# Kernel tuning notes

Measured on AMD Instinct MI355X. Metric: run time of the kernel, lower is better.

## Reference

```python
import jax, jax.numpy as jnp
import numpy as np

B, C, N, K, G = 4, 128, 4096, 9, 4


def setup_inputs() -> dict:
    key = jax.random.key(0)
    ks = jax.random.split(key, 4)
    s = 0.05
    return {
        "features": jax.random.normal(ks[0], (B, C, N, 1), jnp.float32),
        # Attn.linear: Conv2d(2C -> C, 1x1)
        "w_lin": jax.random.normal(ks[1], (C, 2 * C), jnp.float32) * s,
        "b_lin": jnp.zeros((C,), jnp.float32),
        # atten_weight_conv: Linear(C -> K*G)
        "w_aw": jax.random.normal(ks[2], (K * G, C), jnp.float32) * s,
        "b_aw": jnp.zeros((K * G,), jnp.float32),
        # GroupNorm(4, C)
        "gn_g": jnp.ones((C,), jnp.float32),
        "gn_b": jnp.zeros((C,), jnp.float32),
        # conv: Conv2d(C -> C, 1x1) + BatchNorm2d(C)
        "conv_w": jax.random.normal(ks[3], (C, C), jnp.float32) * s,
        "conv_b": jnp.zeros((C,), jnp.float32),
        "bn_g": jnp.ones((C,), jnp.float32),
        "bn_b": jnp.zeros((C,), jnp.float32),
    }


def reference(features, w_lin, b_lin, w_aw, b_aw, gn_g, gn_b, conv_w, conv_b, bn_g, bn_b):
    B, C, N, _ = features.shape
    K, G = 9, 4
    Cg = C // G  # 32 channels per group
    EPS = 1e-5

    x = features[..., 0]                       # [B,C,N]
    # ---- KNN graph (negative squared distance, top-k) ----
    xx = jnp.sum(x * x, axis=1)                # [B,N]
    inner = jnp.einsum('bcn,bcm->bnm', x, x)   # [B,N,N]
    pd = 2.0 * inner - xx[:, :, None] - xx[:, None, :]
    idx = jax.lax.top_k(pd, K)[1]              # [B,N,K]

    # ---- edge feature gather: cat(x, x - x_neighbor) ----
    xt = x.transpose(0, 2, 1)                  # [B,N,C]
    b_ix = jnp.arange(B)[:, None, None]
    nbr = xt[b_ix, idx]                        # [B,N,K,C]
    ctr = jnp.broadcast_to(xt[:, :, None, :], (B, N, K, C))
    edge = jnp.concatenate([ctr, ctr - nbr], axis=-1)   # [B,N,K,2C]

    # ---- Attn.linear (1x1 conv == per-position linear) ----
    feat = jnp.einsum('bnke,ce->bnkc', edge, w_lin) + b_lin  # [B,N,K,C]

    # ---- grouped channel attention (4 groups of 32) ----
    fg = feat.reshape(B, N, K, G, Cg)
    scores = jnp.einsum('bnkgc,bnjgc->bngkj', fg, fg) / np.sqrt(32.0)
    s = jax.nn.softmax(scores, axis=-1)        # [B,N,G,K,K]
    attn = jnp.einsum('bngkj,bnjgc->bngkc', s, jax.nn.elu(fg))  # [B,N,G,K,Cg]

    # ---- attention weights over neighbors ----
    aw = jnp.einsum('bnc,dc->bnd', xt, w_aw) + b_aw          # [B,N,K*G]
    aw = jax.nn.softmax(aw.reshape(B, N, G, K), axis=-1)     # [B,N,G,K]

    # ---- weighted neighbor combine ----
    lf = jnp.einsum('bngk,bngkc->bngc', aw, attn)            # [B,N,G,Cg]
    lf = lf.transpose(0, 2, 3, 1).reshape(B, C, N, 1)        # [B,C,N,1]

    # ---- GroupNorm(4, C) over residual ----
    y = lf + features
    yg = y.reshape(B, G, Cg * N)
    mu = yg.mean(-1, keepdims=True)
    var = yg.var(-1, keepdims=True)
    yn = ((yg - mu) / jnp.sqrt(var + EPS)).reshape(B, C, N, 1)
    yn = yn * gn_g[None, :, None, None] + gn_b[None, :, None, None]

    # ---- 1x1 conv + BatchNorm (training-mode batch stats) + ReLU ----
    z = jnp.einsum('oc,bcnk->bonk', conv_w, yn) + conv_b[None, :, None, None]
    m = z.mean(axis=(0, 2, 3), keepdims=True)
    v = z.var(axis=(0, 2, 3), keepdims=True)
    z = (z - m) / jnp.sqrt(v + EPS) * bn_g[None, :, None, None] + bn_b[None, :, None, None]
    return jax.nn.relu(z)
```

## Files before the change

kernel.cpp:

```cpp
#include <hip/hip_runtime.h>
#include <hip/hip_bf16.h>
#include <cstddef>

#define NPTS 4096
#define CCH  128
#define KNN  9
#define GRP  4
#define BB   4
#define OFF_XT    0u
#define OFF_XX    2097152u
#define OFF_XHI   2113536u
#define OFF_IDX   3162112u
#define OFF_O     3309568u
#define OFF_Y     8159232u
#define OFF_GNP   10256384u
#define OFF_GNA   10387456u
#define OFF_GND   10387968u
#define OFF_WP    10388480u
#define OFF_BIASP 10454016u
#define OFF_BNSUM 10454528u
#define OFF_BNSQ  10454656u
#define OFF_BNSC  10454784u
#define OFF_BNSH  10454912u

using bf16x8 = __attribute__((ext_vector_type(8))) short;
using f32x4  = __attribute__((ext_vector_type(4))) float;

#define CE(a, b) { float _h = fmaxf(a, b); b = fminf(a, b); a = _h; }

#define BMERGE16(s) \
  CE(s[0],s[8])  CE(s[1],s[9])  CE(s[2],s[10]) CE(s[3],s[11]) \
  CE(s[4],s[12]) CE(s[5],s[13]) CE(s[6],s[14]) CE(s[7],s[15]) \
  CE(s[0],s[4])  CE(s[1],s[5])  CE(s[2],s[6])  CE(s[3],s[7])  \
  CE(s[8],s[12]) CE(s[9],s[13]) CE(s[10],s[14]) CE(s[11],s[15]) \
  CE(s[0],s[2])  CE(s[1],s[3])  CE(s[4],s[6])  CE(s[5],s[7])  \
  CE(s[8],s[10]) CE(s[9],s[11]) CE(s[12],s[14]) CE(s[13],s[15]) \
  CE(s[0],s[1])  CE(s[2],s[3])  CE(s[4],s[5])  CE(s[6],s[7])  \
  CE(s[8],s[9])  CE(s[10],s[11]) CE(s[12],s[13]) CE(s[14],s[15])

#define SENT_BITS 0xFF7FF000u

__global__ void k_transpose(const float* __restrict__ x, float* __restrict__ xt,
                            __hip_bfloat16* __restrict__ xhi, float* __restrict__ xx) {
  __shared__ float t[32][33];
  int tx = threadIdx.x, ty = threadIdx.y;
  int n0 = blockIdx.x * 32, c0 = blockIdx.y * 32, b = blockIdx.z;
  float v = x[((size_t)b * CCH + c0 + ty) * NPTS + n0 + tx];
  t[ty][tx] = v;
  __syncthreads();
  float tv = t[tx][ty];
  size_t R = (size_t)b * NPTS + n0 + ty;
  int c = c0 + tx;
  xt[R * CCH + c] = tv;
  int g = c >> 3, w = c & 7;
  int sc = (((g ^ ((n0 + ty) & 15)) << 3) | w);
  xhi[R * CCH + sc] = __float2bfloat16(tv);
  if (ty == 0) {
    float s = 0.f;
    #pragma unroll
    for (int k = 0; k < 32; k++) { float u = t[k][tx]; s += u * u; }
    atomicAdd(&xx[b * NPTS + n0 + tx], s);
  }
}

__device__ __forceinline__ void select_chunk(int c, int wave, int quad,
                                             const f32x4 (&acc)[2][2],
                                             float (&top8)[2][8]) {
  const unsigned cbase = (unsigned)(c * 128 + wave * 32 + quad * 4);
  #pragma unroll
  for (int qt = 0; qt < 2; qt++) {
    float k[8];
    #pragma unroll
    for (int ct = 0; ct < 2; ct++)
      #pragma unroll
      for (int r = 0; r < 4; r++) {
        unsigned u = __float_as_uint(acc[ct][qt][r]);
        k[ct * 4 + r] = __uint_as_float((u & 0xFFFFF000u) |
                                        (cbase + (unsigned)(ct * 16 + r)));
      }
    CE(k[0],k[1]) CE(k[2],k[3]) CE(k[4],k[5]) CE(k[6],k[7])
    CE(k[0],k[2]) CE(k[1],k[3]) CE(k[4],k[6]) CE(k[5],k[7])
    CE(k[1],k[2]) CE(k[5],k[6])
    CE(k[0],k[4]) CE(k[1],k[5]) CE(k[2],k[6]) CE(k[3],k[7])
    CE(k[2],k[4]) CE(k[3],k[5])
    CE(k[1],k[2]) CE(k[3],k[4]) CE(k[5],k[6])
    float t[8];
    #pragma unroll
    for (int i = 0; i < 8; i++) t[i] = fmaxf(top8[qt][i], k[7 - i]);
    CE(t[0],t[4]) CE(t[1],t[5]) CE(t[2],t[6]) CE(t[3],t[7])
    CE(t[0],t[2]) CE(t[1],t[3]) CE(t[4],t[6]) CE(t[5],t[7])
    CE(t[0],t[1]) CE(t[2],t[3]) CE(t[4],t[5]) CE(t[6],t[7])
    #pragma unroll
    for (int i = 0; i < 8; i++) top8[qt][i] = t[i];
  }
}

__device__ __forceinline__ void load_chunk(const short* __restrict__ xb,
                                           const int (&aoff)[4], int c,
                                           bf16x8 (&af)[2][4]) {
  const short* cb = xb + c * (128 * CCH);
  #pragma unroll
  for (int ks = 0; ks < 4; ks++) {
    af[0][ks] = *(const bf16x8*)(cb + aoff[ks]);
    af[1][ks] = *(const bf16x8*)(cb + 2048 + aoff[ks]);
  }
}

__launch_bounds__(256, 4)
__global__ void k_knn(const short* __restrict__ xhi, const float* __restrict__ xx,
                      float* __restrict__ cand) {
  __shared__ short Qs[32 * 136];
  __shared__ float XXs[2048];
  const int tid = threadIdx.x;
  const int wave = tid >> 6, lane = tid & 63;
  const int quad = lane >> 4, m = lane & 15;
  const int b = blockIdx.y;
  const int q0 = blockIdx.x * 32;
  const int z = blockIdx.z;
  const int ch0 = z * 16;
  const short* xb = xhi + (size_t)b * NPTS * CCH;
  const float* xxb = xx + (b << 12);

  {
    int f = tid;
    #pragma unroll
    for (int it = 0; it < 2; it++, f += 256) {
      int row = f >> 4, s = f & 15;
      bf16x8 v = *(const bf16x8*)(xb + (size_t)(q0 + row) * CCH + s * 8);
      int g = s ^ (row & 15);
      *(bf16x8*)&Qs[row * 136 + g * 8] = v;
    }
    const float4* src4 = (const float4*)(xxb + ch0 * 128);
    float4* dst4 = (float4*)XXs;
    #pragma unroll
    for (int j = 0; j < 2; j++) {
      float4 v = src4[tid * 2 + j];
      dst4[tid * 2 + j] = make_float4(-0.5f * v.x, -0.5f * v.y, -0.5f * v.z, -0.5f * v.w);
    }
  }

  int aoff[4];
  #pragma unroll
  for (int ks = 0; ks < 4; ks++)
    aoff[ks] = (wave * 32 + m) * CCH + (((ks * 4 + quad) ^ m) * 8);

  float top8[2][8];
  #pragma unroll
  for (int qt = 0; qt < 2; qt++)
    #pragma unroll
    for (int p = 0; p < 8; p++) top8[qt][p] = __uint_as_float(SENT_BITS);

  f32x4 acc[2][2];
  bf16x8 bufA[2][4], bufB[2][4];

  unsigned qoff = (unsigned)(m * 272 + quad * 16);
  const unsigned xbase = (unsigned)(wave * 128 + quad * 16);

  load_chunk(xb, aoff, ch0, bufA);
  __syncthreads();

  auto mfma_lds = [&](const bf16x8 (&af)[2][4], int crel) {
    unsigned xo = xbase + (unsigned)crel * 512u;
    f32x4 ci0 = *(const f32x4*)((const char*)XXs + xo);
    f32x4 ci1 = *(const f32x4*)((const char*)XXs + xo + 64);
    acc[0][0] = ci0; acc[0][1] = ci0; acc[1][0] = ci1; acc[1][1] = ci1;
    #pragma unroll
    for (int ks = 0; ks < 4; ks++) {
      bf16x8 qv0 = *(const bf16x8*)((const char*)Qs + qoff + ks * 64);
      bf16x8 qv1 = *(const bf16x8*)((const char*)Qs + qoff + 4352 + ks * 64);
      acc[0][0] = __builtin_amdgcn_mfma_f32_16x16x32_bf16(af[0][ks], qv0, acc[0][0], 0, 0, 0);
      acc[0][1] = __builtin_amdgcn_mfma_f32_16x16x32_bf16(af[0][ks], qv1, acc[0][1], 0, 0, 0);
      acc[1][0] = __builtin_amdgcn_mfma_f32_16x16x32_bf16(af[1][ks], qv0, acc[1][0], 0, 0, 0);
      acc[1][1] = __builtin_amdgcn_mfma_f32_16x16x32_bf16(af[1][ks], qv1, acc[1][1], 0, 0, 0);
    }
  };

  for (int c = ch0; c < ch0 + 16; c += 2) {
    load_chunk(xb, aoff, c + 1, bufB);
    if (c > ch0) select_chunk(c - 1, wave, quad, acc, top8);
    asm volatile("" : "+v"(qoff));
    mfma_lds(bufA, c - ch0);
    if (c + 2 < ch0 + 16) load_chunk(xb, aoff, c + 2, bufA);
    select_chunk(c, wave, quad, acc, top8);
    asm volatile("" : "+v"(qoff));
    mfma_lds(bufB, c + 1 - ch0);
  }
  select_chunk(ch0 + 15, wave, quad, acc, top8);

  #pragma unroll
  for (int qt = 0; qt < 2; qt++) {
    float s[16];
    #pragma unroll
    for (int i = 0; i < 8; i++) {
      s[i] = top8[qt][i];
      s[15 - i] = __shfl_xor(top8[qt][i], 16);
    }
    BMERGE16(s)
    float t[16];
    #pragma unroll
    for (int i = 0; i < 16; i++) t[i] = fmaxf(s[i], __shfl_xor(s[15 - i], 32));
    BMERGE16(t)
    if (quad == 0) {
      int q = q0 + qt * 16 + m;
      float* dst = cand + ((size_t)((b << 12) + q) * 128 + (size_t)(z * 4 + wave) * 16);
      *(float4*)&dst[0]  = make_float4(t[0],  t[1],  t[2],  t[3]);
      *(float4*)&dst[4]  = make_float4(t[4],  t[5],  t[6],  t[7]);
      *(float4*)&dst[8]  = make_float4(t[8],  t[9],  t[10], t[11]);
      *(float4*)&dst[12] = make_float4(t[12], t[13], t[14], t[15]);
    }
  }
}

__launch_bounds__(256)
__global__ void k_rerank(const float* __restrict__ cand, const float* __restrict__ xt,
                         const float* __restrict__ xx, int* __restrict__ idxOut) {
  __shared__ __align__(16) float runS[4][128];
  __shared__ int selS[4][16];
  __shared__ float keyS[4][16];
  int tid = threadIdx.x, wave = tid >> 6, lane = tid & 63;
  int qg = blockIdx.x * 4 + wave;
  int b = qg >> 12;
  const float* src = cand + (size_t)qg * 128;
  if (lane < 32) *(float4*)&runS[wave][lane * 4] = *(const float4*)&src[lane * 4];
  __syncthreads();
  if (lane < 16) {
    float t = runS[wave][lane];
    #pragma unroll
    for (int r = 1; r < 8; r++) {
      t = fmaxf(t, runS[wave][r * 16 + (15 - lane)]);
      #pragma unroll
      for (int d = 8; d >= 1; d >>= 1) {
        float o = __shfl_xor(t, d);
        t = (lane & d) ? fminf(t, o) : fmaxf(t, o);
      }
    }
    selS[wave][lane] = (int)(__float_as_uint(t) & 0xFFFu);
  }
  __syncthreads();
  int cnum = lane >> 2, part = lane & 3;
  int cidx = selS[wave][cnum];
  const float* rq = xt + (size_t)qg * CCH;
  const float* rc = xt + ((size_t)(b << 12) + cidx) * CCH;
  float dot = 0.f;
  #pragma unroll
  for (int j = 0; j < 8; j++) {
    float4 a4 = *(const float4*)&rq[part * 32 + j * 4];
    float4 c4 = *(const float4*)&rc[part * 32 + j * 4];
    dot += a4.x * c4.x + a4.y * c4.y + a4.z * c4.z + a4.w * c4.w;
  }
  dot += __shfl_xor(dot, 1);
  dot += __shfl_xor(dot, 2);
  if (part == 0)
    keyS[wave][cnum] = fmaf(2.f, dot, -xx[(b << 12) + cidx]);
  __syncthreads();
  if (lane < 16) {
    float k = keyS[wave][lane]; int i = selS[wave][lane];
    int r = 0;
    #pragma unroll
    for (int f = 0; f < 16; f++) {
      float fk = keyS[wave][f]; int fi = selS[wave][f];
      r += (fk > k) || (fk == k && fi < i);
    }
    if (r < 9) idxOut[(size_t)qg * 9 + r] = i;
  }
}

__launch_bounds__(256)
__global__ void k_linear(const float* __restrict__ xt, const float* __restrict__ w_lin,
                         const float* __restrict__ b_lin, const float* __restrict__ w_aw,
                         const float* __restrict__ b_aw, float* __restrict__ O) {
  __shared__ __align__(16) float Xs[64 * 132];
  __shared__ __align__(16) float Ws[64 * 132];
  int tid = threadIdx.x;
  int tx = tid & 15, ty = tid >> 4;
  int p0 = blockIdx.x * 64, o0 = blockIdx.y * 64;
  #pragma unroll
  for (int i = 0; i < 8; i++) {
    int flat = tid + i * 256; int r = flat >> 5, c4 = flat & 31;
    *(float4*)&Xs[r * 132 + c4 * 4] = *(const float4*)&xt[(size_t)(p0 + r) * CCH + c4 * 4];
  }
  #pragma unroll
  for (int i = 0; i < 8; i++) {
    int flat = tid + i * 256; int r = flat >> 5, c4 = flat & 31;
    int o = o0 + r; float4 v;
    if (o < 128) {
      float4 a = *(const float4*)&w_lin[(size_t)o * 256 + c4 * 4];
      float4 c = *(const float4*)&w_lin[(size_t)o * 256 + 128 + c4 * 4];
      v = make_float4(a.x + c.x, a.y + c.y, a.z + c.z, a.w + c.w);
    } else if (o < 256) {
      v = *(const float4*)&w_lin[(size_t)(o - 128) * 256 + 128 + c4 * 4];
    } else if (o < 292) {
      v = *(const float4*)&w_aw[(size_t)(o - 256) * 128 + c4 * 4];
    } else v = make_float4(0.f, 0.f, 0.f, 0.f);
    *(float4*)&Ws[r * 132 + c4 * 4] = v;
  }
  __syncthreads();
  float acc[4][4] = {};
  #pragma unroll 2
  for (int kq = 0; kq < 32; kq++) {
    float4 xa[4], wb[4];
    #pragma unroll
    for (int i = 0; i < 4; i++) xa[i] = *(const float4*)&Xs[(ty * 4 + i) * 132 + kq * 4];
    #pragma unroll
    for (int j = 0; j < 4; j++) wb[j] = *(const float4*)&Ws[(tx + 16 * j) * 132 + kq * 4];
    #pragma unroll
    for (int i = 0; i < 4; i++)
      #pragma unroll
      for (int j = 0; j < 4; j++)
        acc[i][j] += xa[i].x * wb[j].x + xa[i].y * wb[j].y + xa[i].z * wb[j].z + xa[i].w * wb[j].w;
  }
  #pragma unroll
  for (int j = 0; j < 4; j++) {
    int o = o0 + tx + 16 * j;
    if (o < 292) {
      float bias = (o < 128) ? b_lin[o] : ((o < 256) ? 0.f : b_aw[o - 256]);
      #pragma unroll
      for (int i = 0; i < 4; i++)
        O[(size_t)(p0 + ty * 4 + i) * 296 + o] = acc[i][j] + bias;
    }
  }
}

__launch_bounds__(256)
__global__ void k_attn(const float* __restrict__ O, const int* __restrict__ idxArr,
                       const float* __restrict__ xt, float* __restrict__ Y,
                       float* __restrict__ gnPart) {
  __shared__ __align__(16) float fF[4][1188];
  __shared__ __align__(16) float scS[4][432];
  __shared__ float awS[4][48];
  __shared__ float w9S[4][48];
  __shared__ int tI[45], tJ[45];
  int tid = threadIdx.x;
  int wave = tid >> 6, l = tid & 63;
  int pos = blockIdx.x * 4 + wave;
  int b = pos >> 12;
  if (tid == 0) {
    int p = 0;
    for (int i = 0; i < 9; i++) for (int j = i; j < 9; j++) { tI[p] = i; tJ[p] = j; p++; }
  }
  int nbr[9];
  const float* Op = O + (size_t)pos * 296;
  #pragma unroll
  for (int k = 0; k < 9; k++) nbr[k] = idxArr[(size_t)pos * 9 + k];
  float2 u = *(const float2*)(Op + 2 * l);
  float* fFw = fF[wave];
  #pragma unroll
  for (int k = 0; k < 9; k++) {
    const float* vp = O + (size_t)((b << 12) + nbr[k]) * 296 + 128;
    float2 vv = *(const float2*)(vp + 2 * l);
    *(float2*)&fFw[k * 132 + 2 * l] = make_float2(u.x - vv.x, u.y - vv.y);
  }
  __syncthreads();
  #pragma unroll
  for (int r = 0; r < 3; r++) {
    int p = r * 64 + l;
    if (p < 180) {
      int g = p / 45, q = p - g * 45;
      int i = tI[q], j = tJ[q];
      const float* fi = fFw + i * 132 + g * 32;
      const float* fj = fFw + j * 132 + g * 32;
      float s = 0.f;
      #pragma unroll
      for (int t8 = 0; t8 < 8; t8++) {
        float4 a4 = *(const float4*)(fi + 4 * t8);
        float4 b4 = *(const float4*)(fj + 4 * t8);
        s += a4.x * b4.x + a4.y * b4.y + a4.z * b4.z + a4.w * b4.w;
      }
      s *= 0.17677669529663687f;
      scS[wave][(g * 9 + i) * 12 + j] = s;
      scS[wave][(g * 9 + j) * 12 + i] = s;
    }
  }
  __syncthreads();
  if (l < 36) {
    int g = l / 9, i = l - g * 9;
    float* rp = &scS[wave][(g * 9 + i) * 12];
    float mx = rp[0];
    #pragma unroll
    for (int j = 1; j < 9; j++) mx = fmaxf(mx, rp[j]);
    float e[9]; float sm = 0.f;
    #pragma unroll
    for (int j = 0; j < 9; j++) { e[j] = __expf(rp[j] - mx); sm += e[j]; }
    float inv = 1.f / sm;
    #pragma unroll
    for (int j = 0; j < 9; j++) rp[j] = e[j] * inv;
  } else if (l < 40) {
    int g = l - 36;
    float a[9]; float mx = -3.4e38f;
    #pragma unroll
    for (int k = 0; k < 9; k++) { a[k] = Op[256 + g * 9 + k]; mx = fmaxf(mx, a[k]); }
    float sm = 0.f;
    #pragma unroll
    for (int k = 0; k < 9; k++) { a[k] = __expf(a[k] - mx); sm += a[k]; }
    float inv = 1.f / sm;
    #pragma unroll
    for (int k = 0; k < 9; k++) awS[wave][g * 12 + k] = a[k] * inv;
  }
  __syncthreads();
  if (l < 36) {
    int g = l / 9, j = l - g * 9;
    float s = 0.f;
    #pragma unroll
    for (int i = 0; i < 9; i++) s += awS[wave][g * 12 + i] * scS[wave][(g * 9 + i) * 12 + j];
    w9S[wave][g * 12 + j] = s;
  }
  __syncthreads();
  int g = l >> 4;
  float w9r[9];
  #pragma unroll
  for (int j = 0; j < 9; j++) w9r[j] = w9S[wave][g * 12 + j];
  int c0 = 2 * l;
  float lf0 = 0.f, lf1 = 0.f;
  #pragma unroll
  for (int j = 0; j < 9; j++) {
    float2 f2 = *(const float2*)&fFw[j * 132 + c0];
    float e0 = f2.x > 0.f ? f2.x : __expf(f2.x) - 1.f;
    float e1 = f2.y > 0.f ? f2.y : __expf(f2.y) - 1.f;
    lf0 += w9r[j] * e0;
    lf1 += w9r[j] * e1;
  }
  float2 xv = *(const float2*)(xt + (size_t)pos * CCH + c0);
  float y0 = lf0 + xv.x, y1 = lf1 + xv.y;
  *(float2*)(Y + (size_t)pos * CCH + c0) = make_float2(y0, y1);
  float s1 = y0 + y1, s2 = y0 * y0 + y1 * y1;
  #pragma unroll
  for (int mm = 1; mm <= 8; mm <<= 1) { s1 += __shfl_xor(s1, mm); s2 += __shfl_xor(s2, mm); }
  if ((l & 15) == 0) {
    gnPart[(size_t)pos * 8 + g * 2]     = s1;
    gnPart[(size_t)pos * 8 + g * 2 + 1] = s2;
  }
}

__global__ void k_gnstats(const float* __restrict__ gnPart,
                          const float* __restrict__ gn_g, const float* __restrict__ gn_b,
                          float* __restrict__ gnA, float* __restrict__ gnD) {
  int bg = blockIdx.x; int b = bg >> 2, g = bg & 3;
  int tid = threadIdx.x;
  float s1 = 0.f, s2 = 0.f;
  for (int r = tid; r < NPTS; r += 256) {
    const float* p = gnPart + (size_t)(b * NPTS + r) * 8 + g * 2;
    s1 += p[0]; s2 += p[1];
  }
  __shared__ float r1[256], r2[256];
  r1[tid] = s1; r2[tid] = s2;
  __syncthreads();
  for (int off = 128; off > 0; off >>= 1) {
    if (tid < off) { r1[tid] += r1[tid + off]; r2[tid] += r2[tid + off]; }
    __syncthreads();
  }
  __shared__ float muS, rsS;
  if (tid == 0) {
    float mu = r1[0] * (1.f / 131072.f);
    float var = r2[0] * (1.f / 131072.f) - mu * mu;
    muS = mu; rsS = 1.f / sqrtf(var + 1e-5f);
  }
  __syncthreads();
  if (tid < 32) {
    int c = g * 32 + tid;
    float a = rsS * gn_g[c];
    gnA[b * 128 + c] = a;
    gnD[b * 128 + c] = gn_b[c] - muS * a;
  }
}

__global__ void k_fold(const float* __restrict__ conv_w, const float* __restrict__ conv_b,
                       const float* __restrict__ gnA, const float* __restrict__ gnD,
                       float* __restrict__ Wp, float* __restrict__ biasp) {
  int b = blockIdx.x; int tid = threadIdx.x;
  __shared__ float dS[128], aS[128];
  if (tid < 128) { dS[tid] = gnD[b * 128 + tid]; aS[tid] = gnA[b * 128 + tid]; }
  __syncthreads();
  for (int f = tid; f < 16384; f += 256)
    Wp[(size_t)b * 16384 + f] = conv_w[f] * aS[f & 127];
  if (tid < 128) {
    float s = conv_b[tid];
    for (int c = 0; c < 128; c++) s += conv_w[tid * 128 + c] * dS[c];
    biasp[b * 128 + tid] = s;
  }
}

__launch_bounds__(256)
__global__ void k_conv(const float* __restrict__ Y, const float* __restrict__ Wp,
                       const float* __restrict__ biasp, float* __restrict__ zpre,
                       float* __restrict__ bnSum, float* __restrict__ bnSq) {
  __shared__ __align__(16) float Ys[64 * 132];
  __shared__ __align__(16) float Ws[64 * 132];
  int tid = threadIdx.x;
  int tx = tid & 15, ty = tid >> 4;
  int n0 = blockIdx.x * 64, o0 = blockIdx.y * 64, b = blockIdx.z;
  #pragma unroll
  for (int i = 0; i < 8; i++) {
    int flat = tid + i * 256; int r = flat >> 5, c4 = flat & 31;
    *(float4*)&Ys[r * 132 + c4 * 4] = *(const float4*)&Y[(size_t)((b << 12) + n0 + r) * CCH + c4 * 4];
    *(float4*)&Ws[r * 132 + c4 * 4] = *(const float4*)&Wp[(size_t)b * 16384 + (size_t)(o0 + r) * 128 + c4 * 4];
  }
  __syncthreads();
  float acc[4][4] = {};
  #pragma unroll 2
  for (int kq = 0; kq < 32; kq++) {
    float4 wa[4], yb[4];
    #pragma unroll
    for (int i = 0; i < 4; i++) wa[i] = *(const float4*)&Ws[(ty * 4 + i) * 132 + kq * 4];
    #pragma unroll
    for (int j = 0; j < 4; j++) yb[j] = *(const float4*)&Ys[(tx + 16 * j) * 132 + kq * 4];
    #pragma unroll
    for (int i = 0; i < 4; i++)
      #pragma unroll
      for (int j = 0; j < 4; j++)
        acc[i][j] += wa[i].x * yb[j].x + wa[i].y * yb[j].y + wa[i].z * yb[j].z + wa[i].w * yb[j].w;
  }
  #pragma unroll
  for (int i = 0; i < 4; i++) {
    int o = o0 + ty * 4 + i;
    float bias = biasp[b * 128 + o];
    float p1 = 0.f, p2 = 0.f;
    #pragma unroll
    for (int j = 0; j < 4; j++) {
      float z = acc[i][j] + bias;
      zpre[(((size_t)((b << 7) + o)) << 12) + n0 + tx + 16 * j] = z;
      p1 += z; p2 += z * z;
    }
    #pragma unroll
    for (int mm = 1; mm <= 8; mm <<= 1) { p1 += __shfl_xor(p1, mm); p2 += __shfl_xor(p2, mm); }
    if (tx == 0) { atomicAdd(&bnSum[o], p1); atomicAdd(&bnSq[o], p2); }
  }
}

__global__ void k_bnfin(const float* __restrict__ bnSum, const float* __restrict__ bnSq,
                        const float* __restrict__ bn_g, const float* __restrict__ bn_b,
                        float* __restrict__ bnScale, float* __restrict__ bnShift) {
  int o = threadIdx.x;
  float m = bnSum[o] * (1.f / 16384.f);
  float v = bnSq[o] * (1.f / 16384.f) - m * m;
  float sc = bn_g[o] / sqrtf(v + 1e-5f);
  bnScale[o] = sc;
  bnShift[o] = bn_b[o] - m * sc;
}

__global__ void k_final(const float* __restrict__ zpre, const float* __restrict__ bnScale,
                        const float* __restrict__ bnShift, float* __restrict__ out) {
  int i4 = blockIdx.x * 256 + threadIdx.x;
  int e = i4 * 4;
  int o = (e >> 12) & 127;
  float4 z = *(const float4*)&zpre[e];
  float sc = bnScale[o], sh = bnShift[o];
  float4 r;
  r.x = fmaxf(fmaf(z.x, sc, sh), 0.f);
  r.y = fmaxf(fmaf(z.y, sc, sh), 0.f);
  r.z = fmaxf(fmaf(z.z, sc, sh), 0.f);
  r.w = fmaxf(fmaf(z.w, sc, sh), 0.f);
  *(float4*)&out[e] = r;
}

extern "C" void kernel_launch(void* const* d_in, const int* in_sizes, int n_in,
                              void* d_out, int out_size, void* d_ws, size_t ws_size,
                              hipStream_t stream) {
  const float* features = (const float*)d_in[0];
  const float* w_lin  = (const float*)d_in[1];
  const float* b_lin  = (const float*)d_in[2];
  const float* w_aw   = (const float*)d_in[3];
  const float* b_aw   = (const float*)d_in[4];
  const float* gn_g   = (const float*)d_in[5];
  const float* gn_b   = (const float*)d_in[6];
  const float* conv_w = (const float*)d_in[7];
  const float* conv_b = (const float*)d_in[8];
  const float* bn_g   = (const float*)d_in[9];
  const float* bn_b   = (const float*)d_in[10];

  float* ws    = (float*)d_ws;
  float* xt    = ws + OFF_XT;
  float* xxp   = ws + OFF_XX;
  __hip_bfloat16* xhip = (__hip_bfloat16*)(ws + OFF_XHI);
  int*   idxp  = (int*)(ws + OFF_IDX);
  float* Op    = ws + OFF_O;
  float* candp = ws + OFF_O;
  float* Yp    = ws + OFF_Y;
  float* gnp   = ws + OFF_GNP;
  float* gnA   = ws + OFF_GNA;
  float* gnD   = ws + OFF_GND;
  float* Wp    = ws + OFF_WP;
  float* biasp = ws + OFF_BIASP;
  float* bnSum = ws + OFF_BNSUM;
  float* bnSq  = ws + OFF_BNSQ;
  float* bnSc  = ws + OFF_BNSC;
  float* bnSh  = ws + OFF_BNSH;
  float* zpre  = xt;

  hipMemsetAsync(xxp, 0, NPTS * BB * sizeof(float), stream);
  hipMemsetAsync(bnSum, 0, 256 * sizeof(float), stream);

  k_transpose<<<dim3(128, 4, 4), dim3(32, 32), 0, stream>>>(features, xt, xhip, xxp);
  k_knn<<<dim3(128, 4, 2), 256, 0, stream>>>((const short*)xhip, xxp, candp);
  k_rerank<<<4096, 256, 0, stream>>>(candp, xt, xxp, idxp);
  k_linear<<<dim3(256, 5), 256, 0, stream>>>(xt, w_lin, b_lin, w_aw, b_aw, Op);
  k_attn<<<4096, 256, 0, stream>>>(Op, idxp, xt, Yp, gnp);
  k_gnstats<<<16, 256, 0, stream>>>(gnp, gn_g, gn_b, gnA, gnD);
  k_fold<<<4, 256, 0, stream>>>(conv_w, conv_b, gnA, gnD, Wp, biasp);
  k_conv<<<dim3(64, 2, 4), 256, 0, stream>>>(Yp, Wp, biasp, zpre, bnSum, bnSq);
  k_bnfin<<<1, 128, 0, stream>>>(bnSum, bnSq, bn_g, bn_b, bnSc, bnSh);
  k_final<<<2048, 256, 0, stream>>>(zpre, bnSc, bnSh, (float*)d_out);
}
```

Before: 272.6 us.

## Move linear and conv GEMMs to bf16 MFMA with bf16 operands

Replaces the FP32 LDS-tiled SIMT GEMMs in k_linear and k_conv with bf16 MFMA 16x16x32 instructions that read fragments straight from global memory. A new prep kernel packs the combined linear weights to bf16, k_linear reuses the already swizzled bf16 copy of x, and k_attn now writes Y as bf16 for k_conv. The aim is to cut FP32 FMA work and halve intermediate bandwidth. In exchange the linear and conv outputs carry bf16 rounding error, and the fragment loads no longer go through LDS.

```diff
diff --git a/kernel.cpp b/kernel.cpp
--- a/kernel.cpp
+++ b/kernel.cpp
@@ -22,6 +22,9 @@
 #define OFF_BNSQ  10454656u
 #define OFF_BNSC  10454784u
 #define OFF_BNSH  10454912u
+#define OFF_WLB   10455040u
+#define OFF_B320  10475520u
+#define OFF_WPB   10475840u
 
 using bf16x8 = __attribute__((ext_vector_type(8))) short;
 using f32x4  = __attribute__((ext_vector_type(4))) float;
@@ -39,6 +42,11 @@
   CE(s[8],s[9])  CE(s[10],s[11]) CE(s[12],s[13]) CE(s[14],s[15])
 
 #define SENT_BITS 0xFF7FF000u
+
+__device__ __forceinline__ unsigned short f2bf(float v) {
+  __hip_bfloat16 h = __float2bfloat16(v);
+  return *reinterpret_cast<unsigned short*>(&h);
+}
 
 __global__ void k_transpose(const float* __restrict__ x, float* __restrict__ xt,
                             __hip_bfloat16* __restrict__ xhi, float* __restrict__ xx) {
@@ -265,65 +273,58 @@
   }
 }
 
+__global__ void k_wlinprep(const float* __restrict__ w_lin, const float* __restrict__ b_lin,
+                           const float* __restrict__ w_aw, const float* __restrict__ b_aw,
+                           unsigned short* __restrict__ wlb, float* __restrict__ biasB) {
+  int tid = blockIdx.x * 256 + threadIdx.x;
+  int o = tid >> 7, c = tid & 127;
+  float v;
+  if (o < 128)      v = w_lin[(size_t)o * 256 + c] + w_lin[(size_t)o * 256 + 128 + c];
+  else if (o < 256) v = w_lin[(size_t)(o - 128) * 256 + 128 + c];
+  else if (o < 292) v = w_aw[(size_t)(o - 256) * 128 + c];
+  else              v = 0.f;
+  wlb[tid] = f2bf(v);
+  if (tid < 320)
+    biasB[tid] = (tid < 128) ? b_lin[tid] : ((tid >= 256 && tid < 292) ? b_aw[tid - 256] : 0.f);
+}
+
 __launch_bounds__(256)
-__global__ void k_linear(const float* __restrict__ xt, const float* __restrict__ w_lin,
-                         const float* __restrict__ b_lin, const float* __restrict__ w_aw,
-                         const float* __restrict__ b_aw, float* __restrict__ O) {
-  __shared__ __align__(16) float Xs[64 * 132];
-  __shared__ __align__(16) float Ws[64 * 132];
-  int tid = threadIdx.x;
-  int tx = tid & 15, ty = tid >> 4;
-  int p0 = blockIdx.x * 64, o0 = blockIdx.y * 64;
-  #pragma unroll
-  for (int i = 0; i < 8; i++) {
-    int flat = tid + i * 256; int r = flat >> 5, c4 = flat & 31;
-    *(float4*)&Xs[r * 132 + c4 * 4] = *(const float4*)&xt[(size_t)(p0 + r) * CCH + c4 * 4];
-  }
-  #pragma unroll
-  for (int i = 0; i < 8; i++) {
-    int flat = tid + i * 256; int r = flat >> 5, c4 = flat & 31;
-    int o = o0 + r; float4 v;
-    if (o < 128) {
-      float4 a = *(const float4*)&w_lin[(size_t)o * 256 + c4 * 4];
-      float4 c = *(const float4*)&w_lin[(size_t)o * 256 + 128 + c4 * 4];
-      v = make_float4(a.x + c.x, a.y + c.y, a.z + c.z, a.w + c.w);
-    } else if (o < 256) {
-      v = *(const float4*)&w_lin[(size_t)(o - 128) * 256 + 128 + c4 * 4];
-    } else if (o < 292) {
-      v = *(const float4*)&w_aw[(size_t)(o - 256) * 128 + c4 * 4];
-    } else v = make_float4(0.f, 0.f, 0.f, 0.f);
-    *(float4*)&Ws[r * 132 + c4 * 4] = v;
-  }
-  __syncthreads();
-  float acc[4][4] = {};
-  #pragma unroll 2
-  for (int kq = 0; kq < 32; kq++) {
-    float4 xa[4], wb[4];
-    #pragma unroll
-    for (int i = 0; i < 4; i++) xa[i] = *(const float4*)&Xs[(ty * 4 + i) * 132 + kq * 4];
-    #pragma unroll
-    for (int j = 0; j < 4; j++) wb[j] = *(const float4*)&Ws[(tx + 16 * j) * 132 + kq * 4];
-    #pragma unroll
-    for (int i = 0; i < 4; i++)
-      #pragma unroll
-      for (int j = 0; j < 4; j++)
-        acc[i][j] += xa[i].x * wb[j].x + xa[i].y * wb[j].y + xa[i].z * wb[j].z + xa[i].w * wb[j].w;
-  }
-  #pragma unroll
-  for (int j = 0; j < 4; j++) {
-    int o = o0 + tx + 16 * j;
-    if (o < 292) {
-      float bias = (o < 128) ? b_lin[o] : ((o < 256) ? 0.f : b_aw[o - 256]);
-      #pragma unroll
-      for (int i = 0; i < 4; i++)
-        O[(size_t)(p0 + ty * 4 + i) * 296 + o] = acc[i][j] + bias;
+__global__ void k_linear(const short* __restrict__ xhi, const short* __restrict__ wlb,
+                         const float* __restrict__ biasB, float* __restrict__ O) {
+  const int tid = threadIdx.x;
+  const int wave = tid >> 6, lane = tid & 63;
+  const int quad = lane >> 4, m = lane & 15;
+  const int p0 = blockIdx.x * 64;
+  const int ob = blockIdx.y * 64 + wave * 16;
+  const short* arow = wlb + (size_t)(ob + m) * 128;
+  float4 bias = *(const float4*)&biasB[ob + quad * 4];
+  f32x4 acc[4];
+  #pragma unroll
+  for (int pt = 0; pt < 4; pt++) { acc[pt][0] = bias.x; acc[pt][1] = bias.y; acc[pt][2] = bias.z; acc[pt][3] = bias.w; }
+  #pragma unroll
+  for (int ks = 0; ks < 4; ks++) {
+    bf16x8 a = *(const bf16x8*)(arow + (ks * 4 + quad) * 8);
+    #pragma unroll
+    for (int pt = 0; pt < 4; pt++) {
+      int row = p0 + pt * 16 + m;
+      int slot = (ks * 4 + quad) ^ m;
+      bf16x8 bfr = *(const bf16x8*)(xhi + (size_t)row * 128 + slot * 8);
+      acc[pt] = __builtin_amdgcn_mfma_f32_16x16x32_bf16(a, bfr, acc[pt], 0, 0, 0);
+    }
+  }
+  if (ob + quad * 4 < 292) {
+    #pragma unroll
+    for (int pt = 0; pt < 4; pt++) {
+      int p = p0 + pt * 16 + m;
+      *(float4*)&O[(size_t)p * 296 + ob + quad * 4] =
+          make_float4(acc[pt][0], acc[pt][1], acc[pt][2], acc[pt][3]);
     }
   }
 }
 
 __launch_bounds__(256)
 __global__ void k_attn(const float* __restrict__ O, const int* __restrict__ idxArr,
-                       const float* __restrict__ xt, float* __restrict__ Y,
+                       const float* __restrict__ xt, __hip_bfloat16* __restrict__ Y,
                        float* __restrict__ gnPart) {
   __shared__ __align__(16) float fF[4][1188];
   __shared__ __align__(16) float scS[4][432];
@@ -421,7 +422,9 @@
   }
   float2 xv = *(const float2*)(xt + (size_t)pos * CCH + c0);
   float y0 = lf0 + xv.x, y1 = lf1 + xv.y;
-  *(float2*)(Y + (size_t)pos * CCH + c0) = make_float2(y0, y1);
+  unsigned short us0 = f2bf(y0), us1 = f2bf(y1);
+  unsigned upak = (unsigned)us0 | ((unsigned)us1 << 16);
+  *(unsigned*)((unsigned short*)Y + (size_t)pos * CCH + c0) = upak;
   float s1 = y0 + y1, s2 = y0 * y0 + y1 * y1;
   #pragma unroll
   for (int mm = 1; mm <= 8; mm <<= 1) { s1 += __shfl_xor(s1, mm); s2 += __shfl_xor(s2, mm); }
@@ -465,13 +468,13 @@
 
 __global__ void k_fold(const float* __restrict__ conv_w, const float* __restrict__ conv_b,
                        const float* __restrict__ gnA, const float* __restrict__ gnD,
-                       float* __restrict__ Wp, float* __restrict__ biasp) {
+                       unsigned short* __restrict__ Wpb, float* __restrict__ biasp) {
   int b = blockIdx.x; int tid = threadIdx.x;
   __shared__ float dS[128], aS[128];
   if (tid < 128) { dS[tid] = gnD[b * 128 + tid]; aS[tid] = gnA[b * 128 + tid]; }
   __syncthreads();
   for (int f = tid; f < 16384; f += 256)
-    Wp[(size_t)b * 16384 + f] = conv_w[f] * aS[f & 127];
+    Wpb[(size_t)b * 16384 + f] = f2bf(conv_w[f] * aS[f & 127]);
   if (tid < 128) {
     float s = conv_b[tid];
     for (int c = 0; c < 128; c++) s += conv_w[tid * 128 + c] * dS[c];
@@ -480,49 +483,51 @@
 }
 
 __launch_bounds__(256)
-__global__ void k_conv(const float* __restrict__ Y, const float* __restrict__ Wp,
+__global__ void k_conv(const short* __restrict__ Ybf, const short* __restrict__ Wpb,
                        const float* __restrict__ biasp, float* __restrict__ zpre,
                        float* __restrict__ bnSum, float* __restrict__ bnSq) {
-  __shared__ __align__(16) float Ys[64 * 132];
-  __shared__ __align__(16) float Ws[64 * 132];
-  int tid = threadIdx.x;
-  int tx = tid & 15, ty = tid >> 4;
-  int n0 = blockIdx.x * 64, o0 = blockIdx.y * 64, b = blockIdx.z;
-  #pragma unroll
-  for (int i = 0; i < 8; i++) {
-    int flat = tid + i * 256; int r = flat >> 5, c4 = flat & 31;
-    *(float4*)&Ys[r * 132 + c4 * 4] = *(const float4*)&Y[(size_t)((b << 12) + n0 + r) * CCH + c4 * 4];
-    *(float4*)&Ws[r * 132 + c4 * 4] = *(const float4*)&Wp[(size_t)b * 16384 + (size_t)(o0 + r) * 128 + c4 * 4];
-  }
-  __syncthreads();
-  float acc[4][4] = {};
-  #pragma unroll 2
-  for (int kq = 0; kq < 32; kq++) {
-    float4 wa[4], yb[4];
-    #pragma unroll
-    for (int i = 0; i < 4; i++) wa[i] = *(const float4*)&Ws[(ty * 4 + i) * 132 + kq * 4];
-    #pragma unroll
-    for (int j = 0; j < 4; j++) yb[j] = *(const float4*)&Ys[(tx + 16 * j) * 132 + kq * 4];
-    #pragma unroll
-    for (int i = 0; i < 4; i++)
-      #pragma unroll
-      for (int j = 0; j < 4; j++)
-        acc[i][j] += wa[i].x * yb[j].x + wa[i].y * yb[j].y + wa[i].z * yb[j].z + wa[i].w * yb[j].w;
-  }
-  #pragma unroll
-  for (int i = 0; i < 4; i++) {
-    int o = o0 + ty * 4 + i;
-    float bias = biasp[b * 128 + o];
-    float p1 = 0.f, p2 = 0.f;
-    #pragma unroll
-    for (int j = 0; j < 4; j++) {
-      float z = acc[i][j] + bias;
-      zpre[(((size_t)((b << 7) + o)) << 12) + n0 + tx + 16 * j] = z;
-      p1 += z; p2 += z * z;
-    }
-    #pragma unroll
-    for (int mm = 1; mm <= 8; mm <<= 1) { p1 += __shfl_xor(p1, mm); p2 += __shfl_xor(p2, mm); }
-    if (tx == 0) { atomicAdd(&bnSum[o], p1); atomicAdd(&bnSq[o], p2); }
+  const int tid = threadIdx.x;
+  const int wave = tid >> 6, lane = tid & 63;
+  const int quad = lane >> 4, m = lane & 15;
+  const int n0 = blockIdx.x * 64, b = blockIdx.z;
+  const int obase = blockIdx.y * 64 + wave * 16;
+  const short* arow = Wpb + (size_t)b * 16384 + (size_t)(obase + m) * 128;
+  float4 bias = *(const float4*)&biasp[b * 128 + obase + quad * 4];
+  f32x4 acc[4];
+  #pragma unroll
+  for (int pt = 0; pt < 4; pt++) { acc[pt][0] = bias.x; acc[pt][1] = bias.y; acc[pt][2] = bias.z; acc[pt][3] = bias.w; }
+  #pragma unroll
+  for (int ks = 0; ks < 4; ks++) {
+    bf16x8 a = *(const bf16x8*)(arow + (ks * 4 + quad) * 8);
+    #pragma unroll
+    for (int pt = 0; pt < 4; pt++) {
+      int n = n0 + pt * 16 + m;
+      bf16x8 bfr = *(const bf16x8*)(Ybf + ((size_t)((b << 12) + n)) * 128 + (ks * 4 + quad) * 8);
+      acc[pt] = __builtin_amdgcn_mfma_f32_16x16x32_bf16(a, bfr, acc[pt], 0, 0, 0);
+    }
+  }
+  float p1[4] = {0.f, 0.f, 0.f, 0.f}, p2[4] = {0.f, 0.f, 0.f, 0.f};
+  #pragma unroll
+  for (int pt = 0; pt < 4; pt++) {
+    int n = n0 + pt * 16 + m;
+    #pragma unroll
+    for (int r = 0; r < 4; r++) {
+      float z = acc[pt][r];
+      zpre[(((size_t)((b << 7) + obase + quad * 4 + r)) << 12) + n] = z;
+      p1[r] += z; p2[r] += z * z;
+    }
+  }
+  #pragma unroll
+  for (int r = 0; r < 4; r++) {
+    #pragma unroll
+    for (int d = 1; d <= 8; d <<= 1) { p1[r] += __shfl_xor(p1[r], d); p2[r] += __shfl_xor(p2[r], d); }
+  }
+  if (m == 0) {
+    #pragma unroll
+    for (int r = 0; r < 4; r++) {
+      atomicAdd(&bnSum[obase + quad * 4 + r], p1[r]);
+      atomicAdd(&bnSq[obase + quad * 4 + r], p2[r]);
+    }
   }
 }
 
@@ -574,29 +579,33 @@
   int*   idxp  = (int*)(ws + OFF_IDX);
   float* Op    = ws + OFF_O;
   float* candp = ws + OFF_O;
-  float* Yp    = ws + OFF_Y;
+  __hip_bfloat16* Ybf = (__hip_bfloat16*)(ws + OFF_Y);
   float* gnp   = ws + OFF_GNP;
   float* gnA   = ws + OFF_GNA;
   float* gnD   = ws + OFF_GND;
-  float* Wp    = ws + OFF_WP;
   float* biasp = ws + OFF_BIASP;
   float* bnSum = ws + OFF_BNSUM;
   float* bnSq  = ws + OFF_BNSQ;
   float* bnSc  = ws + OFF_BNSC;
   float* bnSh  = ws + OFF_BNSH;
+  unsigned short* wlbp = (unsigned short*)(ws + OFF_WLB);
+  float* biasB = ws + OFF_B320;
+  unsigned short* wpbp = (unsigned short*)(ws + OFF_WPB);
   float* zpre  = xt;
 
   hipMemsetAsync(xxp, 0, NPTS * BB * sizeof(float), stream);
   hipMemsetAsync(bnSum, 0, 256 * sizeof(float), stream);
 
   k_transpose<<<dim3(128, 4, 4), dim3(32, 32), 0, stream>>>(features, xt, xhip, xxp);
+  k_wlinprep<<<160, 256, 0, stream>>>(w_lin, b_lin, w_aw, b_aw, wlbp, biasB);
   k_knn<<<dim3(128, 4, 2), 256, 0, stream>>>((const short*)xhip, xxp, candp);
   k_rerank<<<4096, 256, 0, stream>>>(candp, xt, xxp, idxp);
-  k_linear<<<dim3(256, 5), 256, 0, stream>>>(xt, w_lin, b_lin, w_aw, b_aw, Op);
-  k_attn<<<4096, 256, 0, stream>>>(Op, idxp, xt, Yp, gnp);
+  k_linear<<<dim3(256, 5), 256, 0, stream>>>((const short*)xhip, (const short*)wlbp, biasB, Op);
+  k_attn<<<4096, 256, 0, stream>>>(Op, idxp, xt, Ybf, gnp);
   k_gnstats<<<16, 256, 0, stream>>>(gnp, gn_g, gn_b, gnA, gnD);
-  k_fold<<<4, 256, 0, stream>>>(conv_w, conv_b, gnA, gnD, Wp, biasp);
-  k_conv<<<dim3(64, 2, 4), 256, 0, stream>>>(Yp, Wp, biasp, zpre, bnSum, bnSq);
+  k_fold<<<4, 256, 0, stream>>>(conv_w, conv_b, gnA, gnD, wpbp, biasp);
+  k_conv<<<dim3(64, 2, 4), 256, 0, stream>>>((const short*)Ybf, (const short*)wpbp, biasp,
+                                             zpre, bnSum, bnSq);
   k_bnfin<<<1, 128, 0, stream>>>(bnSum, bnSq, bn_g, bn_b, bnSc, bnSh);
   k_final<<<2048, 256, 0, stream>>>(zpre, bnSc, bnSh, (float*)d_out);
 }
```

Measured after the change: 254.1 us. 6.8% less time.
